# Kernel tuning notes

Hardware: AMD Instinct MI355X
Metric: run time of the kernel (lower is better)

Reference implementation:

```python
import jax, jax.numpy as jnp
import numpy as np

N, D, H, C, E = 16384, 768, 768, 2, 20

def setup_inputs() -> dict:
    key = jax.random.key(0)
    k1, k2, k3, k4, k5, k6 = jax.random.split(key, 6)
    return {
        "embeddings": jax.random.normal(k1, (N, D), dtype=jnp.float32),
        "component_idx": jax.random.randint(k2, (N,), 0, E, dtype=jnp.int64),
        "W1": jax.random.normal(k3, (E, D, H), dtype=jnp.float32) * (1.0 / np.sqrt(D)),
        "b1": jnp.zeros((E, H), dtype=jnp.float32),
        "W2": jax.random.normal(k4, (E, H, C), dtype=jnp.float32) * (1.0 / np.sqrt(H)),
        "b2": jnp.zeros((E, C), dtype=jnp.float32),
    }

def reference(embeddings, component_idx, W1, b1, W2, b2):
    # Each token n goes through expert component_idx[n]:
    #   y = relu(x @ W1[e] + b1[e]) @ W2[e] + b2[e]
    # The torch module's mask/cat/argsort reassembly is mathematically a
    # per-token select of its own expert's output at the original position.
    # Dense-expert formulation (standard jax MoE fallback), then gather.
    h = jax.nn.relu(jnp.einsum('nd,edh->enh', embeddings, W1) + b1[:, None, :])  # [E,N,H]
    y = jnp.einsum('enh,ehc->enc', h, W2) + b2[:, None, :]                        # [E,N,C]
    n_idx = jnp.arange(embeddings.shape[0])
    return y[component_idx, n_idx]  # [N,C]
```

## Files before the change

### kernel.cpp

```cpp
#include <hip/hip_runtime.h>

#define N_D 768
#define N_H 768
#define N_C 2
#define N_E 20
#define MT 128
#define NT 128
#define BK 32
#define KT (N_D / BK)
#define MAX_TILES 160
#define ROWB (N_D * 2)

typedef __attribute__((ext_vector_type(8))) short short8;
typedef __attribute__((ext_vector_type(4))) float f32x4;

__device__ __forceinline__ unsigned short f2bf(float f) {
  unsigned u = __builtin_bit_cast(unsigned, f);
  u += 0x7FFFu + ((u >> 16) & 1u);
  return (unsigned short)(u >> 16);
}

#define GLD_LDS16(gp, lp)                                                        \
  __builtin_amdgcn_global_load_lds(                                              \
      (const __attribute__((address_space(1))) void*)(gp),                       \
      (__attribute__((address_space(3))) void*)(lp), 16, 0, 0)


__global__ __launch_bounds__(256) void k_hist(const int* __restrict__ cidx,
                                              int* __restrict__ counts, int n) {
  __shared__ int lc[N_E];
  if (threadIdx.x < N_E) lc[threadIdx.x] = 0;
  __syncthreads();
  for (int i = blockIdx.x * blockDim.x + threadIdx.x; i < n;
       i += gridDim.x * blockDim.x) {
    int e = cidx[i];
    e = e < 0 ? 0 : (e >= N_E ? N_E - 1 : e);
    atomicAdd(&lc[e], 1);
  }
  __syncthreads();
  if (threadIdx.x < N_E) atomicAdd(&counts[threadIdx.x], lc[threadIdx.x]);
}

__global__ void k_scan(const int* __restrict__ counts, int* __restrict__ offsets,
                       int* __restrict__ cursor, int* __restrict__ tiles,
                       int* __restrict__ numTiles) {
  if (threadIdx.x == 0) {
    int run = 0, t = 0;
    for (int e = 0; e < N_E; ++e) {
      offsets[e] = run;
      cursor[e] = run;
      int nt = (counts[e] + MT - 1) / MT;
      for (int m = 0; m < nt && t < MAX_TILES; ++m) tiles[t++] = (e << 8) | m;
      run += counts[e];
    }
    *numTiles = t;
  }
}

__global__ __launch_bounds__(256) void k_scatter(const int* __restrict__ cidx,
                                                 int* __restrict__ cursor,
                                                 int* __restrict__ sorted, int n) {
  __shared__ int lc[N_E];
  __shared__ int lbase[N_E];
  int tid = threadIdx.x;
  if (tid < N_E) lc[tid] = 0;
  __syncthreads();
  int i = blockIdx.x * blockDim.x + tid;
  int e = 0, p = 0;
  if (i < n) {
    e = cidx[i];
    e = e < 0 ? 0 : (e >= N_E ? N_E - 1 : e);
    p = atomicAdd(&lc[e], 1);
  }
  __syncthreads();
  if (tid < N_E) lbase[tid] = atomicAdd(&cursor[tid], lc[tid]);
  __syncthreads();
  if (i < n) sorted[lbase[e] + p] = i;
}


__global__ __launch_bounds__(192) void k_gather(const float* __restrict__ emb,
                                                const int* __restrict__ sorted,
                                                unsigned short* __restrict__ Xg,
                                                int n) {
  int row = blockIdx.x;
  int j = threadIdx.x;
  ushort4 o;
  if (row < n) {
    float4 v = ((const float4*)(emb + (size_t)sorted[row] * N_D))[j];
    o.x = f2bf(v.x);
    o.y = f2bf(v.y);
    o.z = f2bf(v.z);
    o.w = f2bf(v.w);
  } else {
    o.x = o.y = o.z = o.w = 0;
  }
  ((ushort4*)(Xg + (size_t)row * N_D))[j] = o;
}


__global__ __launch_bounds__(256) void k_w1_cvt(const float* __restrict__ W1,
                                                unsigned short* __restrict__ W1t) {
  __shared__ float tile[64][65];
  int e = blockIdx.z, h0 = blockIdx.x * 64, d0 = blockIdx.y * 64;
  const float* src = W1 + (size_t)e * N_D * N_H;
  unsigned short* dst = W1t + (size_t)e * N_H * N_D;
  int tx = threadIdx.x & 15, ty = threadIdx.x >> 4;
  for (int s = 0; s < 4; ++s) {
    int d = s * 16 + ty;
    float4 v = *(const float4*)&src[(size_t)(d0 + d) * N_H + h0 + tx * 4];
    tile[d][tx * 4 + 0] = v.x;
    tile[d][tx * 4 + 1] = v.y;
    tile[d][tx * 4 + 2] = v.z;
    tile[d][tx * 4 + 3] = v.w;
  }
  __syncthreads();
  int px = threadIdx.x & 7, py = threadIdx.x >> 3;
  for (int s = 0; s < 2; ++s) {
    int h = s * 32 + py;
    short8 v;
    for (int j = 0; j < 8; ++j)
      v[j] = (short)f2bf(tile[px * 8 + j][h]);
    *(short8*)&dst[(size_t)(h0 + h) * N_D + d0 + px * 8] = v;
  }
}


__global__ __launch_bounds__(256, 2) void k_gemm(
    const unsigned short* __restrict__ Xg, const unsigned short* __restrict__ W1t,
    const float* __restrict__ b1, const float* __restrict__ W2,
    const float* __restrict__ b2, const int* __restrict__ sorted,
    const int* __restrict__ counts, const int* __restrict__ offsets,
    const int* __restrict__ tiles, const int* __restrict__ numTiles,
    float* __restrict__ out) {
  if ((int)blockIdx.y >= *numTiles) return;
  const int tv = tiles[blockIdx.y];
  const int e = tv >> 8;
  const int m0 = (tv & 255) * MT;
  const int off = offsets[e];
  const int cnt_rel = counts[e] - m0;
  const int n0 = blockIdx.x * NT;

  __shared__ unsigned short lA[2][MT * BK];
  __shared__ unsigned short lB[2][NT * BK];

  const int tid = threadIdx.x;
  const int wid = tid >> 6, lane = tid & 63;
  const int wm = (wid >> 1) * 64, wn = (wid & 1) * 64;
  const int quad = lane >> 4, lm = lane & 15;

  const int R0 = wid * 32 + lm;
  const char* agp = (const char*)Xg + (size_t)(off + m0 + R0) * ROWB + quad * 16;
  const char* bgp = (const char*)W1t + (size_t)e * N_H * ROWB +
                    (size_t)(n0 + R0) * ROWB + quad * 16;
  unsigned short* lap[2] = {&lA[0][(wid * 32) * BK], &lA[1][(wid * 32) * BK]};
  unsigned short* lbp[2] = {&lB[0][(wid * 32) * BK], &lB[1][(wid * 32) * BK]};

#define ISSUE_BATCH(kk, b)                                                       \
  do {                                                                           \
    const char* a_ = agp + (kk)*64;                                              \
    const char* b_ = bgp + (kk)*64;                                              \
    GLD_LDS16(a_, lap[b]);                                                       \
    GLD_LDS16(a_ + 16 * ROWB, lap[b] + 16 * BK);                                 \
    GLD_LDS16(b_, lbp[b]);                                                       \
    GLD_LDS16(b_ + 16 * ROWB, lbp[b] + 16 * BK);                                 \
  } while (0)

  f32x4 acc[4][4] = {};

  ISSUE_BATCH(0, 0);
  ISSUE_BATCH(1, 1);

  const int fa = quad * 128 + lm * 8;

  for (int kt = 0; kt < KT; ++kt) {
    const int cur = kt & 1;
    asm volatile("s_waitcnt vmcnt(4)\n\ts_barrier" ::: "memory");
    short8 af[4], bfr[4];
    for (int i = 0; i < 4; ++i)
      af[i] = *(const short8*)&lA[cur][((wm >> 4) + i) * 512 + fa];
    for (int j = 0; j < 4; ++j)
      bfr[j] = *(const short8*)&lB[cur][((wn >> 4) + j) * 512 + fa];
    asm volatile("s_waitcnt lgkmcnt(0)\n\ts_barrier" ::: "memory");
    int kk = kt + 2;
    if (kk >= KT) kk -= KT;
    ISSUE_BATCH(kk, cur);
    for (int i = 0; i < 4; ++i)
      for (int j = 0; j < 4; ++j)
        acc[i][j] =
            __builtin_amdgcn_mfma_f32_16x16x32_bf16(af[i], bfr[j], acc[i][j], 0, 0, 0);
  }

  float y0[4][4], y1[4][4];
  for (int i = 0; i < 4; ++i)
    for (int r = 0; r < 4; ++r) y0[i][r] = y1[i][r] = 0.f;

  for (int j = 0; j < 4; ++j) {
    int col = n0 + wn + j * 16 + lm;
    float bias = b1[e * N_H + col];
    float2 w2 = *(const float2*)&W2[((size_t)e * N_H + col) * N_C];
    for (int i = 0; i < 4; ++i) {
      f32x4 a = acc[i][j];
      for (int r = 0; r < 4; ++r) {
        float h = a[r] + bias;
        h = h > 0.f ? h : 0.f;
        y0[i][r] += h * w2.x;
        y1[i][r] += h * w2.y;
      }
    }
  }
  for (int s = 1; s < 16; s <<= 1) {
    for (int i = 0; i < 4; ++i)
      for (int r = 0; r < 4; ++r) {
        y0[i][r] += __shfl_xor(y0[i][r], s, 64);
        y1[i][r] += __shfl_xor(y1[i][r], s, 64);
      }
  }
  if (lm == 0) {
    const bool add_bias = (n0 == 0) && (wn == 0);
    float bb0 = add_bias ? b2[e * N_C + 0] : 0.f;
    float bb1 = add_bias ? b2[e * N_C + 1] : 0.f;
    for (int i = 0; i < 4; ++i) {
      for (int r = 0; r < 4; ++r) {
        int mrel = wm + i * 16 + quad * 4 + r;
        if (mrel < cnt_rel) {
          int token = sorted[off + m0 + mrel];
          atomicAdd(&out[(size_t)token * N_C + 0], y0[i][r] + bb0);
          atomicAdd(&out[(size_t)token * N_C + 1], y1[i][r] + bb1);
        }
      }
    }
  }
}


extern "C" void kernel_launch(void* const* d_in, const int* in_sizes, int n_in,
                              void* d_out, int out_size, void* d_ws, size_t ws_size,
                              hipStream_t stream) {
  const float* emb = (const float*)d_in[0];
  const int* cidx = (const int*)d_in[1];
  const float* W1 = (const float*)d_in[2];
  const float* b1 = (const float*)d_in[3];
  const float* W2 = (const float*)d_in[4];
  const float* b2 = (const float*)d_in[5];
  float* out = (float*)d_out;
  const int n = in_sizes[1];

  char* ws = (char*)d_ws;
  int* counts = (int*)ws;
  int* offsets = (int*)(ws + 128);
  int* cursor = (int*)(ws + 256);
  int* numTiles = (int*)(ws + 384);
  int* tiles = (int*)(ws + 512);
  int* sorted = (int*)(ws + 2048);
  size_t sorted_bytes = ((size_t)n * 4 + 255) & ~(size_t)255;
  unsigned short* Xg = (unsigned short*)(ws + 2048 + sorted_bytes);
  int pcap = n + MT;
  unsigned short* W1t = Xg + (size_t)pcap * N_D;

  hipMemsetAsync(d_ws, 0, 2048, stream);
  hipMemsetAsync(d_out, 0, (size_t)out_size * sizeof(float), stream);
  int nb = (n + 255) / 256;
  k_hist<<<nb, 256, 0, stream>>>(cidx, counts, n);
  k_scan<<<1, 64, 0, stream>>>(counts, offsets, cursor, tiles, numTiles);
  k_scatter<<<nb, 256, 0, stream>>>(cidx, cursor, sorted, n);
  k_gather<<<pcap, 192, 0, stream>>>(emb, sorted, Xg, n);
  k_w1_cvt<<<dim3(N_H / 64, N_D / 64, N_E), 256, 0, stream>>>(W1, W1t);
  k_gemm<<<dim3(N_H / NT, MAX_TILES), 256, 0, stream>>>(
      Xg, W1t, b1, W2, b2, sorted, counts, offsets, tiles, numTiles, out);
}
```

Measured before the change: 222.5 us.

## Triple-buffer GEMM loads, remap blocks per XCD, parallelize tile scan

The grouped GEMM kernel moves from double to triple buffering of the LDS tiles. The K loop is unrolled with explicit drain steps, which lets the global-to-LDS loads run further ahead of the MFMA work, and occupancy is raised to 3 blocks per CU. The 2D grid becomes a 1D grid that places the N-tiles of one M-tile on the same XCD, so L2 reuse of the activation tile improves. The scan kernel now computes offsets and tile lists with one thread per expert instead of a single serial thread. It drops the MAX_TILES cap on the tile writes, so if the counts ever produced more tiles than that, it would write past the buffer.

```diff
diff --git a/kernel.cpp b/kernel.cpp
--- a/kernel.cpp
+++ b/kernel.cpp
@@ -41,19 +41,23 @@
   if (threadIdx.x < N_E) atomicAdd(&counts[threadIdx.x], lc[threadIdx.x]);
 }
 
-__global__ void k_scan(const int* __restrict__ counts, int* __restrict__ offsets,
-                       int* __restrict__ cursor, int* __restrict__ tiles,
-                       int* __restrict__ numTiles) {
-  if (threadIdx.x == 0) {
-    int run = 0, t = 0;
-    for (int e = 0; e < N_E; ++e) {
-      offsets[e] = run;
-      cursor[e] = run;
-      int nt = (counts[e] + MT - 1) / MT;
-      for (int m = 0; m < nt && t < MAX_TILES; ++m) tiles[t++] = (e << 8) | m;
+__global__ __launch_bounds__(64) void k_scan(const int* __restrict__ counts,
+                                             int* __restrict__ offsets,
+                                             int* __restrict__ cursor,
+                                             int* __restrict__ tiles,
+                                             int* __restrict__ numTiles) {
+  int t = threadIdx.x;
+  if (t < N_E) {
+    int run = 0, trun = 0;
+    for (int e = 0; e < t; ++e) {
       run += counts[e];
+      trun += (counts[e] + MT - 1) / MT;
     }
-    *numTiles = t;
+    offsets[t] = run;
+    cursor[t] = run;
+    int nt = (counts[t] + MT - 1) / MT;
+    for (int m = 0; m < nt; ++m) tiles[trun + m] = (t << 8) | m;
+    if (t == N_E - 1) *numTiles = trun + nt;
   }
 }
 
@@ -126,23 +130,29 @@
 }
 
 
-__global__ __launch_bounds__(256, 2) void k_gemm(
+__global__ __launch_bounds__(256, 3) void k_gemm(
     const unsigned short* __restrict__ Xg, const unsigned short* __restrict__ W1t,
     const float* __restrict__ b1, const float* __restrict__ W2,
     const float* __restrict__ b2, const int* __restrict__ sorted,
     const int* __restrict__ counts, const int* __restrict__ offsets,
     const int* __restrict__ tiles, const int* __restrict__ numTiles,
     float* __restrict__ out) {
-  if ((int)blockIdx.y >= *numTiles) return;
-  const int tv = tiles[blockIdx.y];
+  const int p = blockIdx.x;
+  const int xcd = p & 7;
+  const int t = p >> 3;
+  const int bx = t % 6;
+  const int mth = t / 6;
+  const int mt = xcd + 8 * mth;
+  if (mt >= *numTiles) return;
+  const int tv = tiles[mt];
   const int e = tv >> 8;
   const int m0 = (tv & 255) * MT;
   const int off = offsets[e];
   const int cnt_rel = counts[e] - m0;
-  const int n0 = blockIdx.x * NT;
-
-  __shared__ unsigned short lA[2][MT * BK];
-  __shared__ unsigned short lB[2][NT * BK];
+  const int n0 = bx * NT;
+
+  __shared__ unsigned short lA[3][MT * BK];
+  __shared__ unsigned short lB[3][NT * BK];
 
   const int tid = threadIdx.x;
   const int wid = tid >> 6, lane = tid & 63;
@@ -153,8 +163,10 @@
   const char* agp = (const char*)Xg + (size_t)(off + m0 + R0) * ROWB + quad * 16;
   const char* bgp = (const char*)W1t + (size_t)e * N_H * ROWB +
                     (size_t)(n0 + R0) * ROWB + quad * 16;
-  unsigned short* lap[2] = {&lA[0][(wid * 32) * BK], &lA[1][(wid * 32) * BK]};
-  unsigned short* lbp[2] = {&lB[0][(wid * 32) * BK], &lB[1][(wid * 32) * BK]};
+  unsigned short* lap[3] = {&lA[0][(wid * 32) * BK], &lA[1][(wid * 32) * BK],
+                            &lA[2][(wid * 32) * BK]};
+  unsigned short* lbp[3] = {&lB[0][(wid * 32) * BK], &lB[1][(wid * 32) * BK],
+                            &lB[2][(wid * 32) * BK]};
 
 #define ISSUE_BATCH(kk, b)                                                       \
   do {                                                                           \
@@ -170,25 +182,38 @@
 
   ISSUE_BATCH(0, 0);
   ISSUE_BATCH(1, 1);
+  ISSUE_BATCH(2, 2);
 
   const int fa = quad * 128 + lm * 8;
 
-  for (int kt = 0; kt < KT; ++kt) {
-    const int cur = kt & 1;
+#define GEMM_BODY(kt, cur, DO_ISSUE)                                             \
+  do {                                                                           \
+    short8 af[4], bfr[4];                                                        \
+    for (int i = 0; i < 4; ++i)                                                  \
+      af[i] = *(const short8*)&lA[cur][((wm >> 4) + i) * 512 + fa];              \
+    for (int j = 0; j < 4; ++j)                                                  \
+      bfr[j] = *(const short8*)&lB[cur][((wn >> 4) + j) * 512 + fa];             \
+    asm volatile("s_waitcnt lgkmcnt(0)\n\ts_barrier" ::: "memory");              \
+    if (DO_ISSUE) ISSUE_BATCH((kt) + 3, cur);                                    \
+    for (int i = 0; i < 4; ++i)                                                  \
+      for (int j = 0; j < 4; ++j)                                                \
+        acc[i][j] = __builtin_amdgcn_mfma_f32_16x16x32_bf16(af[i], bfr[j],       \
+                                                            acc[i][j], 0, 0, 0); \
+  } while (0)
+
+#pragma unroll
+  for (int kt = 0; kt < KT - 2; ++kt) {
+    const int cur = kt % 3;
+    asm volatile("s_waitcnt vmcnt(8)\n\ts_barrier" ::: "memory");
+    GEMM_BODY(kt, cur, kt < KT - 3);
+  }
+  {
     asm volatile("s_waitcnt vmcnt(4)\n\ts_barrier" ::: "memory");
-    short8 af[4], bfr[4];
-    for (int i = 0; i < 4; ++i)
-      af[i] = *(const short8*)&lA[cur][((wm >> 4) + i) * 512 + fa];
-    for (int j = 0; j < 4; ++j)
-      bfr[j] = *(const short8*)&lB[cur][((wn >> 4) + j) * 512 + fa];
-    asm volatile("s_waitcnt lgkmcnt(0)\n\ts_barrier" ::: "memory");
-    int kk = kt + 2;
-    if (kk >= KT) kk -= KT;
-    ISSUE_BATCH(kk, cur);
-    for (int i = 0; i < 4; ++i)
-      for (int j = 0; j < 4; ++j)
-        acc[i][j] =
-            __builtin_amdgcn_mfma_f32_16x16x32_bf16(af[i], bfr[j], acc[i][j], 0, 0, 0);
+    GEMM_BODY(KT - 2, (KT - 2) % 3, false);
+  }
+  {
+    asm volatile("s_waitcnt vmcnt(0)\n\ts_barrier" ::: "memory");
+    GEMM_BODY(KT - 1, (KT - 1) % 3, false);
   }
 
   float y0[4][4], y1[4][4];
@@ -266,6 +291,6 @@
   k_scatter<<<nb, 256, 0, stream>>>(cidx, cursor, sorted, n);
   k_gather<<<pcap, 192, 0, stream>>>(emb, sorted, Xg, n);
   k_w1_cvt<<<dim3(N_H / 64, N_D / 64, N_E), 256, 0, stream>>>(W1, W1t);
-  k_gemm<<<dim3(N_H / NT, MAX_TILES), 256, 0, stream>>>(
+  k_gemm<<<8 * 6 * (MAX_TILES / 8), 256, 0, stream>>>(
       Xg, W1t, b1, W2, b2, sorted, counts, offsets, tiles, numTiles, out);
 }
```

Measured after the change: 231.0 us. +3.8%, slower.
